# Kernel tuning notes

Hardware: AMD Instinct MI355X
Metric: run time of the kernel (lower is better)

The kernel has to match this reference:

```python
import jax, jax.numpy as jnp
import numpy as np

N, E, G = 50000, 200000, 2000        # nodes, directed edges, graphs in batch
F_IN, HID, HEADS = 64, 128, 4
DM = HID * HEADS                      # 512, concat GAT output dim
EPS = 1e-5
NEG_SLOPE = 0.2                       # PyG GATConv LeakyReLU slope


def setup_inputs() -> dict:
    key = jax.random.key(0)
    ks = jax.random.split(key, 40)
    rn = lambda k, s, sc: jax.random.normal(k, s, jnp.float32) * sc
    inp = {}
    inp["x"] = rn(ks[0], (N, F_IN), 1.0)
    inp["edge_index"] = jax.random.randint(ks[1], (2, E), 0, N)
    inp["batch"] = jnp.sort(jax.random.randint(ks[2], (N,), 0, G))
    dims = [F_IN, DM, DM]
    for l in range(3):
        d = dims[l]
        inp["W%d" % l] = rn(ks[3 + 4 * l], (d, DM), 1.0 / np.sqrt(d))
        inp["as%d" % l] = rn(ks[4 + 4 * l], (HEADS, HID), 0.1)
        inp["ad%d" % l] = rn(ks[5 + 4 * l], (HEADS, HID), 0.1)
        inp["b%d" % l] = jnp.zeros((DM,), jnp.float32)
        inp["g%d" % l] = jnp.ones((DM,), jnp.float32)
        inp["be%d" % l] = jnp.zeros((DM,), jnp.float32)
    inp["c1w"] = rn(ks[20], (2 * DM, HID), 1.0 / np.sqrt(2 * DM))
    inp["c1b"] = jnp.zeros((HID,), jnp.float32)
    inp["c2w"] = rn(ks[21], (HID, HID // 2), 1.0 / np.sqrt(HID))
    inp["c2b"] = jnp.zeros((HID // 2,), jnp.float32)
    inp["c3w"] = rn(ks[22], (HID // 2, 1), 1.0 / np.sqrt(HID // 2))
    inp["c3b"] = jnp.zeros((1,), jnp.float32)
    return inp


def _gat(x, src, dst, W, a_s, a_d, b):
    """PyG GATConv (heads=HEADS, concat) with self-loops already in src/dst."""
    n = x.shape[0]
    h = (x @ W).reshape(n, HEADS, HID)                     # [N,H,D]
    s_src = jnp.sum(h * a_s, -1)                           # [N,H]
    s_dst = jnp.sum(h * a_d, -1)                           # [N,H]
    e = jax.nn.leaky_relu(s_src[src] + s_dst[dst], NEG_SLOPE)  # [Et,H]
    # segment softmax over incoming edges of each dst node (stable)
    m = jax.lax.stop_gradient(jax.ops.segment_max(e, dst, num_segments=n))
    ex = jnp.exp(e - m[dst])
    alpha = ex / jax.ops.segment_sum(ex, dst, num_segments=n)[dst]
    out = jax.ops.segment_sum(h[src] * alpha[:, :, None], dst, num_segments=n)
    return out.reshape(n, HEADS * HID) + b


def _bn(x, g, b):
    mu = jnp.mean(x, 0)
    var = jnp.var(x, 0)
    return (x - mu) * jax.lax.rsqrt(var + EPS) * g + b


def _forward(x, edge_index, batch, layers, c1w, c1b, c2w, c2b, c3w, c3b):
    loops = jnp.arange(N)
    src = jnp.concatenate([edge_index[0], loops])          # add self-loops
    dst = jnp.concatenate([edge_index[1], loops])
    for (W, a_s, a_d, b, g, be) in layers:
        x = jax.nn.relu(_bn(_gat(x, src, dst, W, a_s, a_d, b), g, be))
    cnt = jax.ops.segment_sum(jnp.ones((N,), x.dtype), batch, num_segments=G)
    mean = jax.ops.segment_sum(x, batch, num_segments=G) / jnp.maximum(cnt, 1.0)[:, None]
    mx = jax.ops.segment_max(x, batch, num_segments=G)
    mx = jnp.where(cnt[:, None] > 0, mx, 0.0)
    h = jnp.concatenate([mean, mx], 1)                     # [G, 2*DM]
    h = jax.nn.relu(h @ c1w + c1b)
    h = jax.nn.relu(h @ c2w + c2b)
    return jax.nn.sigmoid(h @ c3w + c3b).squeeze(-1)       # [G]


def reference(x, edge_index, batch, W0, as0, ad0, b0, g0, be0, W1, as1, ad1, b1, g1, be1, W2, as2, ad2, b2, g2, be2, c1w, c1b, c2w, c2b, c3w, c3b):
    layers = [(W0, as0, ad0, b0, g0, be0), (W1, as1, ad1, b1, g1, be1), (W2, as2, ad2, b2, g2, be2)]
    return _forward(x, edge_index, batch, layers, c1w, c1b, c2w, c2b, c3w, c3b)
```

## Files before the change

kernel.cpp:

```cpp
#include <hip/hip_runtime.h>

#define N_NODES 50000
#define E_EDGES 200000
#define ET_EDGES (E_EDGES + N_NODES)
#define G_GRAPHS 2000
#define F_IN 64
#define HID 128
#define HEADS 4
#define DM 512
#define BN_EPS 1e-5f
#define NEG_SLOPE 0.2f
#define YBLK 391
#define NCHUNK (YBLK / 8)

typedef unsigned short ushort_t;
typedef float floatx4 __attribute__((ext_vector_type(4)));
typedef short short8 __attribute__((ext_vector_type(8)));

__device__ __forceinline__ float b2f(unsigned int u) {
    union { unsigned int i; float f; } v; v.i = u << 16; return v.f;
}
__device__ __forceinline__ ushort_t f2b(float f) {
    union { float f; unsigned int i; } v; v.f = f;
    unsigned int r = v.i + 0x7FFFu + ((v.i >> 16) & 1u);
    return (ushort_t)(r >> 16);
}
__device__ __forceinline__ void unpack8(uint4 v, float* f) {
    f[0] = b2f(v.x & 0xffffu); f[1] = b2f(v.x >> 16);
    f[2] = b2f(v.y & 0xffffu); f[3] = b2f(v.y >> 16);
    f[4] = b2f(v.z & 0xffffu); f[5] = b2f(v.z >> 16);
    f[6] = b2f(v.w & 0xffffu); f[7] = b2f(v.w >> 16);
}

#define XN (N_NODES * F_IN)
#define W0N (F_IN * DM)
#define W1N (DM * DM)
__global__ __launch_bounds__(256) void k_prep(const float* __restrict__ x,
                                              const float* __restrict__ w0,
                                              const float* __restrict__ w1,
                                              const float* __restrict__ w2,
                                              ushort_t* __restrict__ Xb,
                                              ushort_t* __restrict__ Wh0,
                                              ushort_t* __restrict__ Wh1,
                                              ushort_t* __restrict__ Wh2) {
    int t = blockIdx.x * 256 + threadIdx.x;
    if (t < XN) { Xb[t] = f2b(x[t]); return; }
    t -= XN;
    if (t < W0N) {
        int k = t >> 9, n = t & 511;
        Wh0[(size_t)n * F_IN + k] = f2b(w0[t]);
        return;
    }
    t -= W0N;
    if (t < W1N) {
        int k = t >> 9, n = t & 511;
        Wh1[(size_t)n * DM + k] = f2b(w1[t]);
        return;
    }
    t -= W1N;
    if (t < W1N) {
        int k = t >> 9, n = t & 511;
        Wh2[(size_t)n * DM + k] = f2b(w2[t]);
    }
}

__global__ __launch_bounds__(256) void k_mgemm(const ushort_t* __restrict__ A,
                                               const ushort_t* __restrict__ Bh,
                                               const float* __restrict__ stat,
                                               const float* __restrict__ gam,
                                               const float* __restrict__ bet,
                                               const float* __restrict__ a_s,
                                               const float* __restrict__ a_d,
                                               ushort_t* __restrict__ C,
                                               float* __restrict__ ssrc,
                                               float* __restrict__ sdst,
                                               int M, int K) {
    __shared__ __align__(16) ushort_t Ash[128 * 32];
    __shared__ __align__(16) ushort_t Bsh[128 * 32];
    __shared__ float sS[128], sD[128];
    __shared__ float sBs[512], sBt[512];
    int bid = blockIdx.x;
    int head, yb;
    if (bid < NCHUNK * 32) {
        int chunk = bid >> 5, pos = bid & 31;
        yb = chunk * 8 + (pos & 7);
        head = pos >> 3;
    } else {
        int rem = bid - NCHUNK * 32;
        head = rem & 3;
        yb = NCHUNK * 8 + (rem >> 2);
    }
    int m0 = yb * 128, n0 = head * 128;
    int tid = threadIdx.x;
    int lane = tid & 63, wave = tid >> 6;
    int wm = (wave >> 1) * 64, wn = (wave & 1) * 64;
    int r0 = tid >> 2, kv = tid & 3;
    floatx4 acc[4][4] = {};
    bool has_bn = (stat != nullptr);
    if (has_bn) {
        for (int f = tid; f < 512; f += 256) {
            float mu = stat[f] * (1.f / (float)N_NODES);
            float var = fmaxf(stat[512 + f] * (1.f / (float)N_NODES) - mu * mu, 0.f);
            float rs = rsqrtf(var + BN_EPS);
            float sc = gam[f] * rs;
            sBs[f] = sc;
            sBt[f] = bet[f] - mu * sc;
        }
    }
    if (tid < 128) { sS[tid] = 0.f; sD[tid] = 0.f; }
    int rA1 = m0 + r0;      if (rA1 >= M) rA1 = M - 1;
    int rA2 = m0 + r0 + 64; if (rA2 >= M) rA2 = M - 1;
    const ushort_t* pa1 = A + (size_t)rA1 * K + kv * 8;
    const ushort_t* pa2 = A + (size_t)rA2 * K + kv * 8;
    const ushort_t* pbh1 = Bh + (size_t)(n0 + r0) * K + kv * 8;
    const ushort_t* pbh2 = Bh + (size_t)(n0 + r0 + 64) * K + kv * 8;
    int rF = lane & 15, q = lane >> 4;
    int swz = ((q ^ (rF & 3) ^ ((rF >> 2) & 3))) * 8;
    int wswz = ((kv ^ (r0 & 3) ^ ((r0 >> 2) & 3))) * 8;
    uint4 a1 = *(const uint4*)pa1;
    uint4 a2 = *(const uint4*)pa2;
    uint4 b1 = *(const uint4*)pbh1;
    uint4 b2 = *(const uint4*)pbh2;
    for (int k0 = 0; k0 < K; k0 += 32) {
        if (has_bn) {
            float v1[8], v2[8];
            unpack8(a1, v1); unpack8(a2, v2);
            const float* sp = sBs + k0 + kv * 8;
            const float* tp = sBt + k0 + kv * 8;
            unsigned* q1 = (unsigned*)&a1;
            unsigned* q2 = (unsigned*)&a2;
#pragma unroll
            for (int j = 0; j < 4; ++j) {
                float s0 = sp[2 * j], t0 = tp[2 * j];
                float s1 = sp[2 * j + 1], t1 = tp[2 * j + 1];
                unsigned lo1 = f2b(fmaxf(v1[2 * j] * s0 + t0, 0.f));
                unsigned hi1 = f2b(fmaxf(v1[2 * j + 1] * s1 + t1, 0.f));
                unsigned lo2 = f2b(fmaxf(v2[2 * j] * s0 + t0, 0.f));
                unsigned hi2 = f2b(fmaxf(v2[2 * j + 1] * s1 + t1, 0.f));
                q1[j] = lo1 | (hi1 << 16);
                q2[j] = lo2 | (hi2 << 16);
            }
        }
        __syncthreads();
        *(uint4*)&Ash[r0 * 32 + wswz] = a1;
        *(uint4*)&Ash[(r0 + 64) * 32 + wswz] = a2;
        *(uint4*)&Bsh[r0 * 32 + wswz] = b1;
        *(uint4*)&Bsh[(r0 + 64) * 32 + wswz] = b2;
        __syncthreads();
        if (k0 + 32 < K) {
            a1 = *(const uint4*)(pa1 + k0 + 32);
            a2 = *(const uint4*)(pa2 + k0 + 32);
            b1 = *(const uint4*)(pbh1 + k0 + 32);
            b2 = *(const uint4*)(pbh2 + k0 + 32);
        }
        short8 af[4], bf[4];
#pragma unroll
        for (int i = 0; i < 4; ++i)
            af[i] = *(const short8*)&Ash[(wm + i * 16 + rF) * 32 + swz];
#pragma unroll
        for (int j = 0; j < 4; ++j)
            bf[j] = *(const short8*)&Bsh[(wn + j * 16 + rF) * 32 + swz];
#pragma unroll
        for (int i = 0; i < 4; ++i)
#pragma unroll
            for (int j = 0; j < 4; ++j)
                acc[i][j] = __builtin_amdgcn_mfma_f32_16x16x32_bf16(af[i], bf[j], acc[i][j], 0, 0, 0);
    }
    int cr = (lane >> 4) * 4, cc = lane & 15;
#pragma unroll
    for (int i = 0; i < 4; ++i) {
#pragma unroll
        for (int r = 0; r < 4; ++r) {
            int gr = m0 + wm + i * 16 + cr + r;
            if (gr < M) {
#pragma unroll
                for (int j = 0; j < 4; ++j)
                    C[(size_t)gr * DM + n0 + wn + j * 16 + cc] = f2b(acc[i][j][r]);
            }
        }
    }
    float asl_[4], adl_[4];
#pragma unroll
    for (int j = 0; j < 4; ++j) {
        int c = wn + j * 16 + cc;
        asl_[j] = a_s[head * HID + c];
        adl_[j] = a_d[head * HID + c];
    }
#pragma unroll
    for (int i = 0; i < 4; ++i) {
#pragma unroll
        for (int r = 0; r < 4; ++r) {
            float ps = 0.f, pd = 0.f;
#pragma unroll
            for (int j = 0; j < 4; ++j) {
                ps += acc[i][j][r] * asl_[j];
                pd += acc[i][j][r] * adl_[j];
            }
#pragma unroll
            for (int mk = 1; mk < 16; mk <<= 1) {
                ps += __shfl_xor(ps, mk);
                pd += __shfl_xor(pd, mk);
            }
            if (cc == 0) {
                int row = wm + i * 16 + (lane >> 4) * 4 + r;
                atomicAdd(&sS[row], ps);
                atomicAdd(&sD[row], pd);
            }
        }
    }
    __syncthreads();
    if (tid < 128) {
        int gr = m0 + tid;
        if (gr < M) {
            ssrc[gr * 4 + head] = sS[tid];
            sdst[gr * 4 + head] = sD[tid];
        }
    }
}

__global__ void k_degree(const int* __restrict__ ei, int* __restrict__ deg) {
    int e = blockIdx.x * blockDim.x + threadIdx.x;
    if (e >= ET_EDGES) return;
    int d = (e < E_EDGES) ? ei[E_EDGES + e] : (e - E_EDGES);
    atomicAdd(&deg[d], 1);
}

__global__ __launch_bounds__(1024) void k_scan3(const int* __restrict__ deg,
                                                int* __restrict__ offs,
                                                int* __restrict__ cursor) {
    __shared__ int wsum[16];
    __shared__ int carry;
    int t = threadIdx.x;
    int lane = t & 63, wv = t >> 6;
    if (t == 0) carry = 0;
    __syncthreads();
    for (int base = 0; base < N_NODES; base += 1024) {
        int i = base + t;
        int v = (i < N_NODES) ? deg[i] : 0;
        int x = v;
#pragma unroll
        for (int off = 1; off < 64; off <<= 1) {
            int y = __shfl_up(x, off);
            if (lane >= off) x += y;
        }
        if (lane == 63) wsum[wv] = x;
        __syncthreads();
        int wpre = 0;
#pragma unroll
        for (int w = 0; w < 16; ++w) wpre += (w < wv) ? wsum[w] : 0;
        int incl = wpre + x;
        if (i < N_NODES) { int o = carry + (incl - v); offs[i] = o; cursor[i] = o; }
        __syncthreads();
        if (t == 1023) carry += incl;
        __syncthreads();
    }
    if (t == 0) offs[N_NODES] = carry;
}

__global__ void k_scatter(const int* __restrict__ ei, int* __restrict__ cursor,
                          int* __restrict__ csr_src) {
    int e = blockIdx.x * blockDim.x + threadIdx.x;
    if (e >= ET_EDGES) return;
    int sv, d;
    if (e < E_EDGES) { sv = ei[e]; d = ei[E_EDGES + e]; } else { sv = d = e - E_EDGES; }
    int pos = atomicAdd(&cursor[d], 1);
    csr_src[pos] = sv;
}

__global__ void k_gbounds(const int* __restrict__ batch, int* __restrict__ gstart) {
    int i = blockIdx.x * blockDim.x + threadIdx.x;
    if (i >= N_NODES) return;
    int b = batch[i];
    int p = (i == 0) ? -1 : batch[i - 1];
    for (int g = p + 1; g <= b; ++g) gstart[g] = i;
    if (i == N_NODES - 1)
        for (int g = b + 1; g <= G_GRAPHS; ++g) gstart[g] = N_NODES;
}

__global__ __launch_bounds__(256) void k_aggregate(const ushort_t* __restrict__ H,
                                                   const float* __restrict__ ssrc,
                                                   const float* __restrict__ sdst,
                                                   const int* __restrict__ offs,
                                                   const int* __restrict__ csr_src,
                                                   const float* __restrict__ bias,
                                                   ushort_t* __restrict__ out) {
    int wave = threadIdx.x >> 6, lane = threadIdx.x & 63;
    int n = blockIdx.x * 4 + wave;
    if (n >= N_NODES) return;
    int beg = offs[n], end = offs[n + 1];
    int hl = lane >> 4, li = lane & 15;
    float sdh = sdst[n * 4 + hl];
    float m = -1e30f, s = 0.f;
    for (int e = beg + li; e < end; e += 16) {
        float sc = ssrc[csr_src[e] * 4 + hl] + sdh;
        sc = sc > 0.f ? sc : NEG_SLOPE * sc;
        if (sc > m) { s = s * __expf(m - sc) + 1.f; m = sc; }
        else s += __expf(sc - m);
    }
#pragma unroll
    for (int mk = 1; mk < 16; mk <<= 1) {
        float om = __shfl_xor(m, mk), os = __shfl_xor(s, mk);
        float mn = fmaxf(m, om);
        s = s * __expf(m - mn) + os * __expf(om - mn);
        m = mn;
    }
    float mh = m, inv = 1.f / s;
    float acc[8] = { 0.f, 0.f, 0.f, 0.f, 0.f, 0.f, 0.f, 0.f };
    int e = beg;
    for (; e + 4 <= end; e += 4) {
        int sv0 = csr_src[e], sv1 = csr_src[e + 1];
        int sv2 = csr_src[e + 2], sv3 = csr_src[e + 3];
        float s0 = ssrc[sv0 * 4 + hl], s1 = ssrc[sv1 * 4 + hl];
        float s2 = ssrc[sv2 * 4 + hl], s3 = ssrc[sv3 * 4 + hl];
        uint4 h0 = *(const uint4*)&H[(size_t)sv0 * DM + lane * 8];
        uint4 h1 = *(const uint4*)&H[(size_t)sv1 * DM + lane * 8];
        uint4 h2 = *(const uint4*)&H[(size_t)sv2 * DM + lane * 8];
        uint4 h3 = *(const uint4*)&H[(size_t)sv3 * DM + lane * 8];
        s0 += sdh; s0 = s0 > 0.f ? s0 : NEG_SLOPE * s0;
        s1 += sdh; s1 = s1 > 0.f ? s1 : NEG_SLOPE * s1;
        s2 += sdh; s2 = s2 > 0.f ? s2 : NEG_SLOPE * s2;
        s3 += sdh; s3 = s3 > 0.f ? s3 : NEG_SLOPE * s3;
        float a0 = __expf(s0 - mh) * inv, a1 = __expf(s1 - mh) * inv;
        float a2 = __expf(s2 - mh) * inv, a3 = __expf(s3 - mh) * inv;
        float f0[8], f1[8], f2[8], f3[8];
        unpack8(h0, f0); unpack8(h1, f1); unpack8(h2, f2); unpack8(h3, f3);
#pragma unroll
        for (int j = 0; j < 8; ++j)
            acc[j] += a0 * f0[j] + a1 * f1[j] + a2 * f2[j] + a3 * f3[j];
    }
    for (; e < end; ++e) {
        int sv = csr_src[e];
        float sc = ssrc[sv * 4 + hl] + sdh;
        sc = sc > 0.f ? sc : NEG_SLOPE * sc;
        float alpha = __expf(sc - mh) * inv;
        uint4 hv = *(const uint4*)&H[(size_t)sv * DM + lane * 8];
        float f[8]; unpack8(hv, f);
#pragma unroll
        for (int j = 0; j < 8; ++j) acc[j] += alpha * f[j];
    }
    const float* bp = bias + lane * 8;
    float4 b0 = *(const float4*)bp;
    float4 b1 = *(const float4*)(bp + 4);
    acc[0] += b0.x; acc[1] += b0.y; acc[2] += b0.z; acc[3] += b0.w;
    acc[4] += b1.x; acc[5] += b1.y; acc[6] += b1.z; acc[7] += b1.w;
    uint4 ov; unsigned* po = (unsigned*)&ov;
#pragma unroll
    for (int j = 0; j < 4; ++j)
        po[j] = (unsigned)f2b(acc[2 * j]) | ((unsigned)f2b(acc[2 * j + 1]) << 16);
    *(uint4*)&out[(size_t)n * DM + lane * 8] = ov;
}

#define BN_ROWS 125
__global__ __launch_bounds__(256) void k_bnstats(const ushort_t* __restrict__ X,
                                                 float* __restrict__ stat) {
    int t = threadIdx.x;
    int c2 = t * 2;
    int beg = blockIdx.x * BN_ROWS;
    int end = beg + BN_ROWS; if (end > N_NODES) end = N_NODES;
    float s0 = 0.f, s1 = 0.f, q0 = 0.f, q1 = 0.f;
    for (int n = beg; n < end; ++n) {
        unsigned v = *(const unsigned*)&X[(size_t)n * DM + c2];
        float x0 = b2f(v & 0xffffu), x1 = b2f(v >> 16);
        s0 += x0; s1 += x1;
        q0 += x0 * x0; q1 += x1 * x1;
    }
    atomicAdd(&stat[c2], s0);
    atomicAdd(&stat[c2 + 1], s1);
    atomicAdd(&stat[512 + c2], q0);
    atomicAdd(&stat[512 + c2 + 1], q1);
}

__global__ __launch_bounds__(64) void k_pool(const ushort_t* __restrict__ X,
                                             const int* __restrict__ gstart,
                                             const float* __restrict__ stat,
                                             const float* __restrict__ gam,
                                             const float* __restrict__ bet,
                                             float* __restrict__ pool) {
    int g = blockIdx.x, t = threadIdx.x;
    int beg = gstart[g], end = gstart[g + 1];
    float sc[8], sh[8];
#pragma unroll
    for (int j = 0; j < 8; ++j) {
        int f = t * 8 + j;
        float mu = stat[f] * (1.f / (float)N_NODES);
        float var = fmaxf(stat[512 + f] * (1.f / (float)N_NODES) - mu * mu, 0.f);
        float rs = rsqrtf(var + BN_EPS);
        sc[j] = gam[f] * rs;
        sh[j] = bet[f] - mu * sc[j];
    }
    float sum[8] = { 0 }, mx[8];
#pragma unroll
    for (int j = 0; j < 8; ++j) mx[j] = -1e30f;
    for (int nn = beg; nn < end; ++nn) {
        uint4 xv = *(const uint4*)&X[(size_t)nn * DM + t * 8];
        float f[8]; unpack8(xv, f);
#pragma unroll
        for (int j = 0; j < 8; ++j) {
            f[j] = fmaxf(f[j] * sc[j] + sh[j], 0.f);
            sum[j] += f[j]; mx[j] = fmaxf(mx[j], f[j]);
        }
    }
    float cnt = (float)(end - beg);
    float inv = cnt > 0.f ? 1.f / cnt : 0.f;
#pragma unroll
    for (int j = 0; j < 8; ++j) {
        pool[(size_t)g * 1024 + t * 8 + j] = sum[j] * inv;
        pool[(size_t)g * 1024 + 512 + t * 8 + j] = cnt > 0.f ? mx[j] : 0.f;
    }
}

__global__ __launch_bounds__(128) void k_mlp(const float* __restrict__ pool,
                                             const float* __restrict__ c1w,
                                             const float* __restrict__ c1b,
                                             const float* __restrict__ c2w,
                                             const float* __restrict__ c2b,
                                             const float* __restrict__ c3w,
                                             const float* __restrict__ c3b,
                                             float* __restrict__ out) {
    __shared__ float row[1024];
    __shared__ float h1[128];
    __shared__ float h2[64];
    int g = blockIdx.x, t = threadIdx.x;
    for (int i = t; i < 1024; i += 128) row[i] = pool[(size_t)g * 1024 + i];
    __syncthreads();
    float a1 = c1b[t];
#pragma unroll 8
    for (int k = 0; k < 1024; ++k) a1 += row[k] * c1w[k * 128 + t];
    h1[t] = fmaxf(a1, 0.f);
    __syncthreads();
    if (t < 64) {
        float a2 = c2b[t];
#pragma unroll 8
        for (int k = 0; k < 128; ++k) a2 += h1[k] * c2w[k * 64 + t];
        h2[t] = fmaxf(a2, 0.f);
    }
    __syncthreads();
    if (t < 64) {
        float p = h2[t] * c3w[t];
#pragma unroll
        for (int off = 32; off > 0; off >>= 1) p += __shfl_down(p, off);
        if (t == 0) {
            float z = p + c3b[0];
            out[g] = 1.f / (1.f + __expf(-z));
        }
    }
}

extern "C" void kernel_launch(void* const* d_in, const int* in_sizes, int n_in,
                              void* d_out, int out_size, void* d_ws, size_t ws_size,
                              hipStream_t stream) {
    const float* x = (const float*)d_in[0];
    const int* ei = (const int*)d_in[1];
    const int* batch = (const int*)d_in[2];
    const float* c1w = (const float*)d_in[21];
    const float* c1b = (const float*)d_in[22];
    const float* c2w = (const float*)d_in[23];
    const float* c2b = (const float*)d_in[24];
    const float* c3w = (const float*)d_in[25];
    const float* c3b = (const float*)d_in[26];

    char* p = (char*)d_ws;
    auto carve = [&](size_t bytes) -> char* {
        char* r = p; p += (bytes + 255) & ~(size_t)255; return r;
    };
    ushort_t* A      = (ushort_t*)carve((size_t)N_NODES * DM * 2);
    ushort_t* Hb     = (ushort_t*)carve((size_t)N_NODES * DM * 2);
    ushort_t* Xb     = (ushort_t*)carve((size_t)N_NODES * F_IN * 2);
    ushort_t* Wh0    = (ushort_t*)carve((size_t)F_IN * DM * 2);
    ushort_t* Wh1    = (ushort_t*)carve((size_t)DM * DM * 2);
    ushort_t* Wh2    = (ushort_t*)carve((size_t)DM * DM * 2);
    float*    ssrc   = (float*)carve((size_t)N_NODES * 4 * 4);
    float*    sdst   = (float*)carve((size_t)N_NODES * 4 * 4);
    int*      deg    = (int*)carve((size_t)N_NODES * 4);
    int*      offs   = (int*)carve((size_t)(N_NODES + 1) * 4);
    int*      cursor = (int*)carve((size_t)N_NODES * 4);
    int*      csrsrc = (int*)carve((size_t)ET_EDGES * 4);
    float*    bnstat = (float*)carve(3 * 1024 * 4);
    int*      gstart = (int*)carve((size_t)(G_GRAPHS + 1) * 4);
    float*    pool   = (float*)carve((size_t)G_GRAPHS * 1024 * 4);

    hipMemsetAsync(deg, 0, (size_t)N_NODES * 4, stream);
    hipMemsetAsync(bnstat, 0, 3 * 1024 * 4, stream);
    k_degree<<<(ET_EDGES + 255) / 256, 256, 0, stream>>>(ei, deg);
    k_scan3<<<1, 1024, 0, stream>>>(deg, offs, cursor);
    k_scatter<<<(ET_EDGES + 255) / 256, 256, 0, stream>>>(ei, cursor, csrsrc);
    k_gbounds<<<(N_NODES + 255) / 256, 256, 0, stream>>>(batch, gstart);
    {
        int total = XN + W0N + 2 * W1N;
        k_prep<<<(total + 255) / 256, 256, 0, stream>>>(
            x, (const float*)d_in[3], (const float*)d_in[9], (const float*)d_in[15],
            Xb, Wh0, Wh1, Wh2);
    }

    const ushort_t* xin = Xb;
    const ushort_t* Whs[3] = { Wh0, Wh1, Wh2 };
    const float* pstat = nullptr;
    const float* pgam = nullptr;
    const float* pbet = nullptr;
    for (int l = 0; l < 3; ++l) {
        int K = (l == 0) ? F_IN : DM;
        const float* as_ = (const float*)d_in[4 + 6 * l];
        const float* ad_ = (const float*)d_in[5 + 6 * l];
        const float* bia = (const float*)d_in[6 + 6 * l];
        const float* gam = (const float*)d_in[7 + 6 * l];
        const float* bet = (const float*)d_in[8 + 6 * l];

        k_mgemm<<<4 * YBLK, 256, 0, stream>>>(
            xin, Whs[l], pstat, pgam, pbet, as_, ad_, Hb, ssrc, sdst, N_NODES, K);
        k_aggregate<<<(N_NODES + 3) / 4, 256, 0, stream>>>(Hb, ssrc, sdst, offs, csrsrc, bia, A);
        k_bnstats<<<(N_NODES + BN_ROWS - 1) / BN_ROWS, 256, 0, stream>>>(A, bnstat + l * 1024);
        xin = A; pstat = bnstat + l * 1024; pgam = gam; pbet = bet;
    }
    k_pool<<<G_GRAPHS, 64, 0, stream>>>(A, gstart, bnstat + 2 * 1024, pgam, pbet, pool);
    k_mlp<<<G_GRAPHS, 128, 0, stream>>>(pool, c1w, c1b, c2w, c2b, c3w, c3b,
                                        (float*)d_out);
}
```

Baseline: 703.6 us.

## Load GEMM tiles directly into LDS, split BN apply, batch MLP graphs

The GEMM loads A and B tiles straight into LDS with global_load_lds instead of staging through registers. This means the BatchNorm+ReLU that used to be fused into the A-load moves to a separate k_bnapply kernel. The layer buffers ping-pong between two workspaces, and the MLP kernel handles 8 graphs per block to reuse weight loads. In exchange there is an extra full read and write of the activation array per layer and the register prefetch overlap is lost.

```diff
diff --git a/kernel.cpp b/kernel.cpp
--- a/kernel.cpp
+++ b/kernel.cpp
@@ -30,6 +30,11 @@
     f[2] = b2f(v.y & 0xffffu); f[3] = b2f(v.y >> 16);
     f[4] = b2f(v.z & 0xffffu); f[5] = b2f(v.z >> 16);
     f[6] = b2f(v.w & 0xffffu); f[7] = b2f(v.w >> 16);
+}
+__device__ __forceinline__ void glds16(const ushort_t* g, ushort_t* l) {
+    __builtin_amdgcn_global_load_lds(
+        (const __attribute__((address_space(1))) unsigned int*)g,
+        (__attribute__((address_space(3))) unsigned int*)l, 16, 0, 0);
 }
 
 #define XN (N_NODES * F_IN)
@@ -66,9 +71,6 @@
 
 __global__ __launch_bounds__(256) void k_mgemm(const ushort_t* __restrict__ A,
                                                const ushort_t* __restrict__ Bh,
-                                               const float* __restrict__ stat,
-                                               const float* __restrict__ gam,
-                                               const float* __restrict__ bet,
                                                const float* __restrict__ a_s,
                                                const float* __restrict__ a_d,
                                                ushort_t* __restrict__ C,
@@ -78,7 +80,6 @@
     __shared__ __align__(16) ushort_t Ash[128 * 32];
     __shared__ __align__(16) ushort_t Bsh[128 * 32];
     __shared__ float sS[128], sD[128];
-    __shared__ float sBs[512], sBt[512];
     int bid = blockIdx.x;
     int head, yb;
     if (bid < NCHUNK * 32) {
@@ -94,65 +95,31 @@
     int tid = threadIdx.x;
     int lane = tid & 63, wave = tid >> 6;
     int wm = (wave >> 1) * 64, wn = (wave & 1) * 64;
-    int r0 = tid >> 2, kv = tid & 3;
     floatx4 acc[4][4] = {};
-    bool has_bn = (stat != nullptr);
-    if (has_bn) {
-        for (int f = tid; f < 512; f += 256) {
-            float mu = stat[f] * (1.f / (float)N_NODES);
-            float var = fmaxf(stat[512 + f] * (1.f / (float)N_NODES) - mu * mu, 0.f);
-            float rs = rsqrtf(var + BN_EPS);
-            float sc = gam[f] * rs;
-            sBs[f] = sc;
-            sBt[f] = bet[f] - mu * sc;
-        }
-    }
     if (tid < 128) { sS[tid] = 0.f; sD[tid] = 0.f; }
-    int rA1 = m0 + r0;      if (rA1 >= M) rA1 = M - 1;
-    int rA2 = m0 + r0 + 64; if (rA2 >= M) rA2 = M - 1;
-    const ushort_t* pa1 = A + (size_t)rA1 * K + kv * 8;
-    const ushort_t* pa2 = A + (size_t)rA2 * K + kv * 8;
-    const ushort_t* pbh1 = Bh + (size_t)(n0 + r0) * K + kv * 8;
-    const ushort_t* pbh2 = Bh + (size_t)(n0 + r0 + 64) * K + kv * 8;
+    int lrow = lane >> 2, lchunk = lane & 3;
+    int fs = (lrow & 3) ^ ((lrow >> 2) & 3);
+    int schunk = lchunk ^ fs;
+    int ar0 = wave * 16 + lrow;
+    int ar1 = ar0 + 64;
+    int gr0 = m0 + ar0; if (gr0 >= M) gr0 = M - 1;
+    int gr1 = m0 + ar1; if (gr1 >= M) gr1 = M - 1;
+    const ushort_t* gA0 = A + (size_t)gr0 * K + schunk * 8;
+    const ushort_t* gA1 = A + (size_t)gr1 * K + schunk * 8;
+    const ushort_t* gB0 = Bh + (size_t)(n0 + ar0) * K + schunk * 8;
+    const ushort_t* gB1 = Bh + (size_t)(n0 + ar1) * K + schunk * 8;
+    ushort_t* lA0 = &Ash[(wave * 16) * 32];
+    ushort_t* lA1 = &Ash[(wave * 16 + 64) * 32];
+    ushort_t* lB0 = &Bsh[(wave * 16) * 32];
+    ushort_t* lB1 = &Bsh[(wave * 16 + 64) * 32];
     int rF = lane & 15, q = lane >> 4;
     int swz = ((q ^ (rF & 3) ^ ((rF >> 2) & 3))) * 8;
-    int wswz = ((kv ^ (r0 & 3) ^ ((r0 >> 2) & 3))) * 8;
-    uint4 a1 = *(const uint4*)pa1;
-    uint4 a2 = *(const uint4*)pa2;
-    uint4 b1 = *(const uint4*)pbh1;
-    uint4 b2 = *(const uint4*)pbh2;
     for (int k0 = 0; k0 < K; k0 += 32) {
-        if (has_bn) {
-            float v1[8], v2[8];
-            unpack8(a1, v1); unpack8(a2, v2);
-            const float* sp = sBs + k0 + kv * 8;
-            const float* tp = sBt + k0 + kv * 8;
-            unsigned* q1 = (unsigned*)&a1;
-            unsigned* q2 = (unsigned*)&a2;
-#pragma unroll
-            for (int j = 0; j < 4; ++j) {
-                float s0 = sp[2 * j], t0 = tp[2 * j];
-                float s1 = sp[2 * j + 1], t1 = tp[2 * j + 1];
-                unsigned lo1 = f2b(fmaxf(v1[2 * j] * s0 + t0, 0.f));
-                unsigned hi1 = f2b(fmaxf(v1[2 * j + 1] * s1 + t1, 0.f));
-                unsigned lo2 = f2b(fmaxf(v2[2 * j] * s0 + t0, 0.f));
-                unsigned hi2 = f2b(fmaxf(v2[2 * j + 1] * s1 + t1, 0.f));
-                q1[j] = lo1 | (hi1 << 16);
-                q2[j] = lo2 | (hi2 << 16);
-            }
-        }
+        glds16(gA0 + k0, lA0);
+        glds16(gA1 + k0, lA1);
+        glds16(gB0 + k0, lB0);
+        glds16(gB1 + k0, lB1);
         __syncthreads();
-        *(uint4*)&Ash[r0 * 32 + wswz] = a1;
-        *(uint4*)&Ash[(r0 + 64) * 32 + wswz] = a2;
-        *(uint4*)&Bsh[r0 * 32 + wswz] = b1;
-        *(uint4*)&Bsh[(r0 + 64) * 32 + wswz] = b2;
-        __syncthreads();
-        if (k0 + 32 < K) {
-            a1 = *(const uint4*)(pa1 + k0 + 32);
-            a2 = *(const uint4*)(pa2 + k0 + 32);
-            b1 = *(const uint4*)(pbh1 + k0 + 32);
-            b2 = *(const uint4*)(pbh2 + k0 + 32);
-        }
         short8 af[4], bf[4];
 #pragma unroll
         for (int i = 0; i < 4; ++i)
@@ -165,6 +132,7 @@
 #pragma unroll
             for (int j = 0; j < 4; ++j)
                 acc[i][j] = __builtin_amdgcn_mfma_f32_16x16x32_bf16(af[i], bf[j], acc[i][j], 0, 0, 0);
+        __syncthreads();
     }
     int cr = (lane >> 4) * 4, cc = lane & 15;
 #pragma unroll
@@ -215,6 +183,39 @@
             ssrc[gr * 4 + head] = sS[tid];
             sdst[gr * 4 + head] = sD[tid];
         }
+    }
+}
+
+__global__ __launch_bounds__(256) void k_bnapply(const ushort_t* __restrict__ X,
+                                                 const float* __restrict__ stat,
+                                                 const float* __restrict__ gam,
+                                                 const float* __restrict__ bet,
+                                                 ushort_t* __restrict__ Y) {
+    __shared__ float sc[512], sh[512];
+    int t = threadIdx.x;
+    for (int f = t; f < 512; f += 256) {
+        float mu = stat[f] * (1.f / (float)N_NODES);
+        float var = fmaxf(stat[512 + f] * (1.f / (float)N_NODES) - mu * mu, 0.f);
+        float rs = rsqrtf(var + BN_EPS);
+        float s = gam[f] * rs;
+        sc[f] = s;
+        sh[f] = bet[f] - mu * s;
+    }
+    __syncthreads();
+    int c8 = (t & 63) * 8;
+    const float* scp = sc + c8;
+    const float* shp = sh + c8;
+    for (int n = blockIdx.x * 4 + (t >> 6); n < N_NODES; n += gridDim.x * 4) {
+        uint4 v = *(const uint4*)&X[(size_t)n * DM + c8];
+        float fv[8]; unpack8(v, fv);
+        uint4 ov; unsigned* po = (unsigned*)&ov;
+#pragma unroll
+        for (int j = 0; j < 4; ++j) {
+            unsigned lo = f2b(fmaxf(fv[2 * j] * scp[2 * j] + shp[2 * j], 0.f));
+            unsigned hi = f2b(fmaxf(fv[2 * j + 1] * scp[2 * j + 1] + shp[2 * j + 1], 0.f));
+            po[j] = lo | (hi << 16);
+        }
+        *(uint4*)&Y[(size_t)n * DM + c8] = ov;
     }
 }
 
@@ -409,6 +410,7 @@
     }
 }
 
+#define MLP_GPB 8
 __global__ __launch_bounds__(128) void k_mlp(const float* __restrict__ pool,
                                              const float* __restrict__ c1w,
                                              const float* __restrict__ c1b,
@@ -417,31 +419,51 @@
                                              const float* __restrict__ c3w,
                                              const float* __restrict__ c3b,
                                              float* __restrict__ out) {
-    __shared__ float row[1024];
-    __shared__ float h1[128];
-    __shared__ float h2[64];
-    int g = blockIdx.x, t = threadIdx.x;
-    for (int i = t; i < 1024; i += 128) row[i] = pool[(size_t)g * 1024 + i];
+    __shared__ float row[MLP_GPB][1024];
+    __shared__ float h1[MLP_GPB][128];
+    __shared__ float h2s[MLP_GPB][64];
+    int g0 = blockIdx.x * MLP_GPB, t = threadIdx.x;
+#pragma unroll
+    for (int gi = 0; gi < MLP_GPB; ++gi)
+        for (int i = t; i < 1024; i += 128)
+            row[gi][i] = pool[(size_t)(g0 + gi) * 1024 + i];
     __syncthreads();
-    float a1 = c1b[t];
-#pragma unroll 8
-    for (int k = 0; k < 1024; ++k) a1 += row[k] * c1w[k * 128 + t];
-    h1[t] = fmaxf(a1, 0.f);
+    float a1[MLP_GPB];
+#pragma unroll
+    for (int gi = 0; gi < MLP_GPB; ++gi) a1[gi] = c1b[t];
+#pragma unroll 4
+    for (int k = 0; k < 1024; ++k) {
+        float w = c1w[k * 128 + t];
+#pragma unroll
+        for (int gi = 0; gi < MLP_GPB; ++gi) a1[gi] += row[gi][k] * w;
+    }
+#pragma unroll
+    for (int gi = 0; gi < MLP_GPB; ++gi) h1[gi][t] = fmaxf(a1[gi], 0.f);
     __syncthreads();
     if (t < 64) {
-        float a2 = c2b[t];
-#pragma unroll 8
-        for (int k = 0; k < 128; ++k) a2 += h1[k] * c2w[k * 64 + t];
-        h2[t] = fmaxf(a2, 0.f);
+        float a2[MLP_GPB];
+#pragma unroll
+        for (int gi = 0; gi < MLP_GPB; ++gi) a2[gi] = c2b[t];
+#pragma unroll 2
+        for (int k = 0; k < 128; ++k) {
+            float w = c2w[k * 64 + t];
+#pragma unroll
+            for (int gi = 0; gi < MLP_GPB; ++gi) a2[gi] += h1[gi][k] * w;
+        }
+#pragma unroll
+        for (int gi = 0; gi < MLP_GPB; ++gi) h2s[gi][t] = fmaxf(a2[gi], 0.f);
     }
     __syncthreads();
     if (t < 64) {
-        float p = h2[t] * c3w[t];
-#pragma unroll
-        for (int off = 32; off > 0; off >>= 1) p += __shfl_down(p, off);
-        if (t == 0) {
-            float z = p + c3b[0];
-            out[g] = 1.f / (1.f + __expf(-z));
+#pragma unroll
+        for (int gi = 0; gi < MLP_GPB; ++gi) {
+            float p = h2s[gi][t] * c3w[t];
+#pragma unroll
+            for (int off = 32; off > 0; off >>= 1) p += __shfl_down(p, off);
+            if (t == 0) {
+                float z = p + c3b[0];
+                out[g0 + gi] = 1.f / (1.f + __expf(-z));
+            }
         }
     }
 }
@@ -463,8 +485,8 @@
     auto carve = [&](size_t bytes) -> char* {
         char* r = p; p += (bytes + 255) & ~(size_t)255; return r;
     };
-    ushort_t* A      = (ushort_t*)carve((size_t)N_NODES * DM * 2);
-    ushort_t* Hb     = (ushort_t*)carve((size_t)N_NODES * DM * 2);
+    ushort_t* buf0   = (ushort_t*)carve((size_t)N_NODES * DM * 2);
+    ushort_t* buf1   = (ushort_t*)carve((size_t)N_NODES * DM * 2);
     ushort_t* Xb     = (ushort_t*)carve((size_t)N_NODES * F_IN * 2);
     ushort_t* Wh0    = (ushort_t*)carve((size_t)F_IN * DM * 2);
     ushort_t* Wh1    = (ushort_t*)carve((size_t)DM * DM * 2);
@@ -492,11 +514,10 @@
             Xb, Wh0, Wh1, Wh2);
     }
 
-    const ushort_t* xin = Xb;
     const ushort_t* Whs[3] = { Wh0, Wh1, Wh2 };
-    const float* pstat = nullptr;
     const float* pgam = nullptr;
     const float* pbet = nullptr;
+    const ushort_t* in = Xb;
     for (int l = 0; l < 3; ++l) {
         int K = (l == 0) ? F_IN : DM;
         const float* as_ = (const float*)d_in[4 + 6 * l];
@@ -504,14 +525,19 @@
         const float* bia = (const float*)d_in[6 + 6 * l];
         const float* gam = (const float*)d_in[7 + 6 * l];
         const float* bet = (const float*)d_in[8 + 6 * l];
+        ushort_t* h   = (l % 2 == 0) ? buf1 : buf0;
+        ushort_t* agg = (l % 2 == 0) ? buf0 : buf1;
 
         k_mgemm<<<4 * YBLK, 256, 0, stream>>>(
-            xin, Whs[l], pstat, pgam, pbet, as_, ad_, Hb, ssrc, sdst, N_NODES, K);
-        k_aggregate<<<(N_NODES + 3) / 4, 256, 0, stream>>>(Hb, ssrc, sdst, offs, csrsrc, bia, A);
-        k_bnstats<<<(N_NODES + BN_ROWS - 1) / BN_ROWS, 256, 0, stream>>>(A, bnstat + l * 1024);
-        xin = A; pstat = bnstat + l * 1024; pgam = gam; pbet = bet;
-    }
-    k_pool<<<G_GRAPHS, 64, 0, stream>>>(A, gstart, bnstat + 2 * 1024, pgam, pbet, pool);
-    k_mlp<<<G_GRAPHS, 128, 0, stream>>>(pool, c1w, c1b, c2w, c2b, c3w, c3b,
-                                        (float*)d_out);
-}
+            in, Whs[l], as_, ad_, h, ssrc, sdst, N_NODES, K);
+        k_aggregate<<<(N_NODES + 3) / 4, 256, 0, stream>>>(h, ssrc, sdst, offs, csrsrc, bia, agg);
+        k_bnstats<<<(N_NODES + BN_ROWS - 1) / BN_ROWS, 256, 0, stream>>>(agg, bnstat + l * 1024);
+        if (l < 2)
+            k_bnapply<<<2048, 256, 0, stream>>>(agg, bnstat + l * 1024, gam, bet, h);
+        in = h;
+        pgam = gam; pbet = bet;
+    }
+    k_pool<<<G_GRAPHS, 64, 0, stream>>>(buf0, gstart, bnstat + 2 * 1024, pgam, pbet, pool);
+    k_mlp<<<G_GRAPHS / MLP_GPB, 128, 0, stream>>>(pool, c1w, c1b, c2w, c2b, c3w, c3b,
+                                                  (float*)d_out);
+}
```

New measurement: 779.9 us. 1.11x slower.
